# Performance work log

Hardware: AMD Instinct MI355X
Metric: run time of the kernel (lower is better)

Reference implementation:

```python
import jax, jax.numpy as jnp
import numpy as np

BATCH, N_CONCEPTS, EMBED_DIM = 16384, 4096, 64
CURVATURE = 1.0
EPS = 1e-7
BALL_SCALE = 0.05  # keep points inside the Poincare ball (c*||x||^2 < 1)


def setup_inputs() -> dict:
    key = jax.random.key(0)
    k1, k2 = jax.random.split(key)
    embeddings = BALL_SCALE * jax.random.normal(k1, (BATCH, EMBED_DIM), dtype=jnp.float32)
    prototypes = BALL_SCALE * jax.random.normal(k2, (N_CONCEPTS, EMBED_DIM), dtype=jnp.float32)
    return {"embeddings": embeddings, "prototypes": prototypes}


def poincare_pairwise(x, p, c):
    # x: (B, D) points, p: (N, D) prototypes -> (B, N) hyperbolic distances.
    # d(x,y) = (1/sqrt(c)) * acosh(1 + 2c*||x-y||^2 / ((1 - c||x||^2)(1 - c||y||^2)))
    x2 = jnp.sum(x * x, axis=-1)                     # (B,)
    p2 = jnp.sum(p * p, axis=-1)                     # (N,)
    xp = x @ p.T                                     # (B, N) single fused GEMM
    sq = jnp.maximum(x2[:, None] + p2[None, :] - 2.0 * xp, 0.0)  # (B, N)
    denom = jnp.maximum((1.0 - c * x2)[:, None] * (1.0 - c * p2)[None, :], EPS)
    arg = 1.0 + 2.0 * c * sq / denom
    return jnp.arccosh(jnp.maximum(arg, 1.0 + EPS)) / jnp.sqrt(c)


def reference(embeddings, prototypes) -> jnp.ndarray:
    # Vectorized equivalent of the per-concept Python loop over prototypes.
    return poincare_pairwise(embeddings, prototypes, CURVATURE)  # (B, N)
```

## Files before the change

### kernel.cpp

```cpp
#include <hip/hip_runtime.h>
#include <hip/hip_bf16.h>


constexpr int BATCH = 16384;
constexpr int NCON  = 4096;
constexpr int DIM   = 64;
constexpr float LN2 = 0.6931471805599453f;

constexpr size_t WS_EMB   = 0;
constexpr size_t WS_PROTO = (size_t)2 << 20;
constexpr size_t WS_X2    = WS_PROTO + (512u << 10);
constexpr size_t WS_CROW  = WS_X2   + 64u * 1024;
constexpr size_t WS_P2    = WS_CROW + 64u * 1024;
constexpr size_t WS_RP    = WS_P2   + 16u * 1024;

typedef float  f32x4  __attribute__((ext_vector_type(4)));
typedef __bf16 bf16x8 __attribute__((ext_vector_type(8)));

__global__ __launch_bounds__(256)
void prepass_kernel(const float* __restrict__ emb,
                    const float* __restrict__ proto,
                    char* __restrict__ ws)
{
    int gid = blockIdx.x * 256 + threadIdx.x;
    if (gid < 131072) {
        int c = gid;
        int strip = c >> 7, r = c & 127;
        int kk = r >> 6, lane = r & 63;
        int row = strip * 16 + (lane & 15);
        int k0  = kk * 32 + (lane >> 4) * 8;
        const float* src = emb + (size_t)row * DIM + k0;
        f32x4 a = *reinterpret_cast<const f32x4*>(src);
        f32x4 b = *reinterpret_cast<const f32x4*>(src + 4);
        bf16x8 v;
        v[0]=(__bf16)a.x; v[1]=(__bf16)a.y; v[2]=(__bf16)a.z; v[3]=(__bf16)a.w;
        v[4]=(__bf16)b.x; v[5]=(__bf16)b.y; v[6]=(__bf16)b.z; v[7]=(__bf16)b.w;
        *reinterpret_cast<bf16x8*>(ws + WS_EMB + (size_t)c * 16) = v;
    } else if (gid < 163840) {
        int c = gid - 131072;
        int nt = c >> 10, r = c & 1023;
        int pf = r >> 7, rr = r & 127;
        int kk = rr >> 6, lane = rr & 63;
        int row = nt * 128 + pf * 16 + (lane & 15);
        int k0  = kk * 32 + (lane >> 4) * 8;
        const float* src = proto + (size_t)row * DIM + k0;
        f32x4 a = *reinterpret_cast<const f32x4*>(src);
        f32x4 b = *reinterpret_cast<const f32x4*>(src + 4);
        bf16x8 v;
        v[0]=(__bf16)a.x; v[1]=(__bf16)a.y; v[2]=(__bf16)a.z; v[3]=(__bf16)a.w;
        v[4]=(__bf16)b.x; v[5]=(__bf16)b.y; v[6]=(__bf16)b.z; v[7]=(__bf16)b.w;
        *reinterpret_cast<bf16x8*>(ws + WS_PROTO + (size_t)c * 16) = v;
    } else if (gid < 180224) {
        int r = gid - 163840;
        const f32x4* src = reinterpret_cast<const f32x4*>(emb + (size_t)r * DIM);
        float s = 0.0f;
        #pragma unroll
        for (int i = 0; i < 16; ++i) {
            f32x4 v = src[i];
            s += v.x*v.x + v.y*v.y + v.z*v.z + v.w*v.w;
        }
        reinterpret_cast<float*>(ws + WS_X2)[r]   = s;
        reinterpret_cast<float*>(ws + WS_CROW)[r] = 2.0f * __builtin_amdgcn_rcpf(1.0f - s);
    } else if (gid < 184320) {
        int r = gid - 180224;
        const f32x4* src = reinterpret_cast<const f32x4*>(proto + (size_t)r * DIM);
        float s = 0.0f;
        #pragma unroll
        for (int i = 0; i < 16; ++i) {
            f32x4 v = src[i];
            s += v.x*v.x + v.y*v.y + v.z*v.z + v.w*v.w;
        }
        reinterpret_cast<float*>(ws + WS_P2)[r] = s;
        reinterpret_cast<float*>(ws + WS_RP)[r] = __builtin_amdgcn_rcpf(1.0f - s);
    }
}

__global__ __launch_bounds__(256, 4)
void poincare_pairwise_kernel(const char* __restrict__ ws,
                              float* __restrict__ out)
{
    const int tid  = threadIdx.x;
    const int bid  = blockIdx.x;
    const int mg   = bid >> 4;
    const int ng   = bid & 15;
    const int lane = tid & 63;
    const int wid  = tid >> 6;
    const int lr   = lane & 15;
    const int g    = lane >> 4;
    const int strip = mg * 4 + wid;
    const int row   = strip * 16 + lr;

    const bf16x8* ebase = reinterpret_cast<const bf16x8*>(ws + WS_EMB) + (size_t)strip * 128 + lane;
    const bf16x8 xfrag0 = ebase[0];
    const bf16x8 xfrag1 = ebase[64];

    const float x2   = reinterpret_cast<const float*>(ws + WS_X2)[row];
    const float crow = reinterpret_cast<const float*>(ws + WS_CROW)[row];
    float* rowp = out + (size_t)row * NCON;

    #pragma unroll
    for (int t = 0; t < 2; ++t) {
        const int nt = ng * 2 + t;
        const bf16x8* pbase = reinterpret_cast<const bf16x8*>(ws + WS_PROTO) + (size_t)nt * 1024 + lane;

        f32x4 acc[8] = {};
        #pragma unroll
        for (int kk = 0; kk < 2; ++kk) {
            bf16x8 pfrag[8];
            #pragma unroll
            for (int pf = 0; pf < 8; ++pf)
                pfrag[pf] = pbase[(pf * 2 + kk) * 64];
            #pragma unroll
            for (int pf = 0; pf < 8; ++pf)
                acc[pf] = __builtin_amdgcn_mfma_f32_16x16x32_bf16(
                    pfrag[pf], kk ? xfrag1 : xfrag0, acc[pf], 0, 0, 0);
        }

        const float* p2a = reinterpret_cast<const float*>(ws + WS_P2) + nt * 128;
        const float* rpa = reinterpret_cast<const float*>(ws + WS_RP) + nt * 128;
        #pragma unroll
        for (int pf = 0; pf < 8; ++pf) {
            int   col = pf * 16 + g * 4;
            f32x4 p2  = *reinterpret_cast<const f32x4*>(p2a + col);
            f32x4 rp  = *reinterpret_cast<const f32x4*>(rpa + col);
            f32x4 dv;
            #pragma unroll
            for (int j = 0; j < 4; ++j) {
                float sq = fmaxf(x2 + p2[j] - 2.0f * acc[pf][j], 0.0f);
                float tt = sq * (crow * rp[j]);
                float s  = __builtin_amdgcn_sqrtf(tt * (tt + 2.0f));
                dv[j]    = LN2 * __builtin_amdgcn_logf(1.0f + tt + s);
            }
            *reinterpret_cast<f32x4*>(rowp + nt * 128 + col) = dv;
        }
    }
}

extern "C" void kernel_launch(void* const* d_in, const int* in_sizes, int n_in,
                              void* d_out, int out_size, void* d_ws, size_t ws_size,
                              hipStream_t stream) {
    const float* emb   = (const float*)d_in[0];
    const float* proto = (const float*)d_in[1];
    float* out = (float*)d_out;
    char* ws   = (char*)d_ws;

    prepass_kernel<<<720, 256, 0, stream>>>(emb, proto, ws);
    poincare_pairwise_kernel<<<4096, 256, 0, stream>>>(ws, out);
}
```

Measured before the change: 74.80 us.

## Fuse embedding bf16 conversion and norms into main kernel, remap blocks per row strip

Drops the embedding bf16 repack and squared-norm computation from the prepass and instead loads fp32 embeddings directly in the main kernel. Each block converts its lanes' values to bf16 fragments and reduces the row norm with cross-lane shuffles. Work is remapped so each block owns one 16-row strip and each wave sweeps 8 column tiles, which cuts the prepass size and its workspace round-trip. The cost is redundant per-wave embedding loads and conversion, plus a longer per-wave loop with fewer blocks.

```diff
diff --git a/kernel.cpp b/kernel.cpp
--- a/kernel.cpp
+++ b/kernel.cpp
@@ -7,37 +7,20 @@
 constexpr int DIM   = 64;
 constexpr float LN2 = 0.6931471805599453f;
 
-constexpr size_t WS_EMB   = 0;
-constexpr size_t WS_PROTO = (size_t)2 << 20;
-constexpr size_t WS_X2    = WS_PROTO + (512u << 10);
-constexpr size_t WS_CROW  = WS_X2   + 64u * 1024;
-constexpr size_t WS_P2    = WS_CROW + 64u * 1024;
-constexpr size_t WS_RP    = WS_P2   + 16u * 1024;
+constexpr size_t WS_PROTO = 0;
+constexpr size_t WS_P2    = (size_t)512 << 10;
+constexpr size_t WS_RP    = WS_P2 + 16u * 1024;
 
 typedef float  f32x4  __attribute__((ext_vector_type(4)));
 typedef __bf16 bf16x8 __attribute__((ext_vector_type(8)));
 
 __global__ __launch_bounds__(256)
-void prepass_kernel(const float* __restrict__ emb,
-                    const float* __restrict__ proto,
+void prepass_kernel(const float* __restrict__ proto,
                     char* __restrict__ ws)
 {
     int gid = blockIdx.x * 256 + threadIdx.x;
-    if (gid < 131072) {
+    if (gid < 32768) {
         int c = gid;
-        int strip = c >> 7, r = c & 127;
-        int kk = r >> 6, lane = r & 63;
-        int row = strip * 16 + (lane & 15);
-        int k0  = kk * 32 + (lane >> 4) * 8;
-        const float* src = emb + (size_t)row * DIM + k0;
-        f32x4 a = *reinterpret_cast<const f32x4*>(src);
-        f32x4 b = *reinterpret_cast<const f32x4*>(src + 4);
-        bf16x8 v;
-        v[0]=(__bf16)a.x; v[1]=(__bf16)a.y; v[2]=(__bf16)a.z; v[3]=(__bf16)a.w;
-        v[4]=(__bf16)b.x; v[5]=(__bf16)b.y; v[6]=(__bf16)b.z; v[7]=(__bf16)b.w;
-        *reinterpret_cast<bf16x8*>(ws + WS_EMB + (size_t)c * 16) = v;
-    } else if (gid < 163840) {
-        int c = gid - 131072;
         int nt = c >> 10, r = c & 1023;
         int pf = r >> 7, rr = r & 127;
         int kk = rr >> 6, lane = rr & 63;
@@ -50,19 +33,8 @@
         v[0]=(__bf16)a.x; v[1]=(__bf16)a.y; v[2]=(__bf16)a.z; v[3]=(__bf16)a.w;
         v[4]=(__bf16)b.x; v[5]=(__bf16)b.y; v[6]=(__bf16)b.z; v[7]=(__bf16)b.w;
         *reinterpret_cast<bf16x8*>(ws + WS_PROTO + (size_t)c * 16) = v;
-    } else if (gid < 180224) {
-        int r = gid - 163840;
-        const f32x4* src = reinterpret_cast<const f32x4*>(emb + (size_t)r * DIM);
-        float s = 0.0f;
-        #pragma unroll
-        for (int i = 0; i < 16; ++i) {
-            f32x4 v = src[i];
-            s += v.x*v.x + v.y*v.y + v.z*v.z + v.w*v.w;
-        }
-        reinterpret_cast<float*>(ws + WS_X2)[r]   = s;
-        reinterpret_cast<float*>(ws + WS_CROW)[r] = 2.0f * __builtin_amdgcn_rcpf(1.0f - s);
-    } else if (gid < 184320) {
-        int r = gid - 180224;
+    } else if (gid < 36864) {
+        int r = gid - 32768;
         const f32x4* src = reinterpret_cast<const f32x4*>(proto + (size_t)r * DIM);
         float s = 0.0f;
         #pragma unroll
@@ -76,32 +48,48 @@
 }
 
 __global__ __launch_bounds__(256, 4)
-void poincare_pairwise_kernel(const char* __restrict__ ws,
+void poincare_pairwise_kernel(const float* __restrict__ emb,
+                              const char* __restrict__ ws,
                               float* __restrict__ out)
 {
     const int tid  = threadIdx.x;
     const int bid  = blockIdx.x;
-    const int mg   = bid >> 4;
-    const int ng   = bid & 15;
     const int lane = tid & 63;
     const int wid  = tid >> 6;
     const int lr   = lane & 15;
     const int g    = lane >> 4;
-    const int strip = mg * 4 + wid;
-    const int row   = strip * 16 + lr;
+    const int row  = bid * 16 + lr;
 
-    const bf16x8* ebase = reinterpret_cast<const bf16x8*>(ws + WS_EMB) + (size_t)strip * 128 + lane;
-    const bf16x8 xfrag0 = ebase[0];
-    const bf16x8 xfrag1 = ebase[64];
+    const float* esrc = emb + (size_t)row * DIM;
+    f32x4 a0 = *reinterpret_cast<const f32x4*>(esrc + g * 8);
+    f32x4 a1 = *reinterpret_cast<const f32x4*>(esrc + g * 8 + 4);
+    f32x4 b0 = *reinterpret_cast<const f32x4*>(esrc + 32 + g * 8);
+    f32x4 b1 = *reinterpret_cast<const f32x4*>(esrc + 32 + g * 8 + 4);
 
-    const float x2   = reinterpret_cast<const float*>(ws + WS_X2)[row];
-    const float crow = reinterpret_cast<const float*>(ws + WS_CROW)[row];
+    bf16x8 xf0, xf1;
+    xf0[0]=(__bf16)a0.x; xf0[1]=(__bf16)a0.y; xf0[2]=(__bf16)a0.z; xf0[3]=(__bf16)a0.w;
+    xf0[4]=(__bf16)a1.x; xf0[5]=(__bf16)a1.y; xf0[6]=(__bf16)a1.z; xf0[7]=(__bf16)a1.w;
+    xf1[0]=(__bf16)b0.x; xf1[1]=(__bf16)b0.y; xf1[2]=(__bf16)b0.z; xf1[3]=(__bf16)b0.w;
+    xf1[4]=(__bf16)b1.x; xf1[5]=(__bf16)b1.y; xf1[6]=(__bf16)b1.z; xf1[7]=(__bf16)b1.w;
+
+    float ss = a0.x*a0.x + a0.y*a0.y + a0.z*a0.z + a0.w*a0.w
+             + a1.x*a1.x + a1.y*a1.y + a1.z*a1.z + a1.w*a1.w
+             + b0.x*b0.x + b0.y*b0.y + b0.z*b0.z + b0.w*b0.w
+             + b1.x*b1.x + b1.y*b1.y + b1.z*b1.z + b1.w*b1.w;
+    ss += __shfl_xor(ss, 16);
+    ss += __shfl_xor(ss, 32);
+    const float x2   = ss;
+    const float crow = 2.0f * __builtin_amdgcn_rcpf(1.0f - x2);
     float* rowp = out + (size_t)row * NCON;
 
-    #pragma unroll
-    for (int t = 0; t < 2; ++t) {
-        const int nt = ng * 2 + t;
-        const bf16x8* pbase = reinterpret_cast<const bf16x8*>(ws + WS_PROTO) + (size_t)nt * 1024 + lane;
+    const bf16x8* pimg = reinterpret_cast<const bf16x8*>(ws + WS_PROTO);
+    const float*  p2a  = reinterpret_cast<const float*>(ws + WS_P2);
+    const float*  rpa  = reinterpret_cast<const float*>(ws + WS_RP);
+
+    #pragma unroll 2
+    for (int t = 0; t < 8; ++t) {
+        const int nt = wid * 8 + t;
+        const bf16x8* pbase = pimg + (size_t)nt * 1024 + lane;
 
         f32x4 acc[8] = {};
         #pragma unroll
@@ -113,14 +101,13 @@
             #pragma unroll
             for (int pf = 0; pf < 8; ++pf)
                 acc[pf] = __builtin_amdgcn_mfma_f32_16x16x32_bf16(
-                    pfrag[pf], kk ? xfrag1 : xfrag0, acc[pf], 0, 0, 0);
+                    pfrag[pf], kk ? xf1 : xf0, acc[pf], 0, 0, 0);
         }
 
-        const float* p2a = reinterpret_cast<const float*>(ws + WS_P2) + nt * 128;
-        const float* rpa = reinterpret_cast<const float*>(ws + WS_RP) + nt * 128;
+        const int cbase = nt * 128;
         #pragma unroll
         for (int pf = 0; pf < 8; ++pf) {
-            int   col = pf * 16 + g * 4;
+            int   col = cbase + pf * 16 + g * 4;
             f32x4 p2  = *reinterpret_cast<const f32x4*>(p2a + col);
             f32x4 rp  = *reinterpret_cast<const f32x4*>(rpa + col);
             f32x4 dv;
@@ -131,7 +118,7 @@
                 float s  = __builtin_amdgcn_sqrtf(tt * (tt + 2.0f));
                 dv[j]    = LN2 * __builtin_amdgcn_logf(1.0f + tt + s);
             }
-            *reinterpret_cast<f32x4*>(rowp + nt * 128 + col) = dv;
+            *reinterpret_cast<f32x4*>(rowp + col) = dv;
         }
     }
 }
@@ -144,6 +131,6 @@
     float* out = (float*)d_out;
     char* ws   = (char*)d_ws;
 
-    prepass_kernel<<<720, 256, 0, stream>>>(emb, proto, ws);
-    poincare_pairwise_kernel<<<4096, 256, 0, stream>>>(ws, out);
+    prepass_kernel<<<144, 256, 0, stream>>>(proto, ws);
+    poincare_pairwise_kernel<<<BATCH / 16, 256, 0, stream>>>(emb, ws, out);
 }
```

New measurement: 80.49 us. 1.08x slower.
